# Optimization experiments

Measured on AMD Instinct MI355X. Metric: run time of the kernel, lower is better.

The kernel has to match this reference:

```python
import math
import jax, jax.numpy as jnp
import numpy as np

B, C_IN, S = 8, 1024, 2048
KEY_DIM, OUT_DIM = 512, 1024


def setup_inputs() -> dict:
    key = jax.random.key(0)
    ks = jax.random.split(key, 7)
    scale_in = 1.0 / math.sqrt(C_IN)
    return {
        "x": jax.random.normal(ks[0], (B, C_IN, S), dtype=jnp.float32),
        # Conv1d kernel_size=1 weights stored as (out_ch, in_ch)
        "wq": jax.random.uniform(ks[1], (KEY_DIM, C_IN), jnp.float32, -scale_in, scale_in),
        "bq": jax.random.uniform(ks[2], (KEY_DIM,), jnp.float32, -scale_in, scale_in),
        "wk": jax.random.uniform(ks[3], (KEY_DIM, C_IN), jnp.float32, -scale_in, scale_in),
        "bk": jax.random.uniform(ks[4], (KEY_DIM,), jnp.float32, -scale_in, scale_in),
        "wv": jax.random.uniform(ks[5], (OUT_DIM, C_IN), jnp.float32, -scale_in, scale_in),
        "bv": jax.random.uniform(ks[6], (OUT_DIM,), jnp.float32, -scale_in, scale_in),
    }


def reference(x, wq, bq, wk, bk, wv, bv):
    # x: (B, C, S). 1x1 Conv1d == per-position linear over channels.
    q = jnp.einsum("bcs,kc->bsk", x, wq) + bq            # (B, S, K)
    k = jnp.einsum("bcs,kc->bks", x, wk) + bk[:, None]   # (B, K, S)
    v = jnp.einsum("bcs,oc->bso", x, wv) + bv            # (B, S, O)
    scores = jnp.einsum("bsk,bkt->bst", q, k) / math.sqrt(KEY_DIM)  # (B, S, S)
    attention = jax.nn.softmax(scores, axis=-1)
    # out = (attn @ v) then transpose(1,2) -> (B, O, S)
    out = jnp.einsum("bst,bto->bos", attention, v)
    return out
```

## Files before the change

### kernel.cpp

```cpp
#include <hip/hip_runtime.h>
#include <hip/hip_bf16.h>
#include <math.h>

#define SEQ 2048
#define CIN 1024
#define KD  512
#define OD  1024
#define NB  8

typedef __attribute__((ext_vector_type(8))) short bf16x8;
typedef __attribute__((ext_vector_type(4))) float f32x4;

__device__ __forceinline__ short f2bs(float f) {
  unsigned u = __float_as_uint(f);
  unsigned r = (u + 0x7FFFu + ((u >> 16) & 1u)) >> 16;
  return (short)(r & 0xFFFFu);
}

__device__ __forceinline__ float bs2f(short s) {
  return __uint_as_float(((unsigned)(unsigned short)s) << 16);
}

__device__ __forceinline__ f32x4 mfma16(bf16x8 a, bf16x8 b, f32x4 c) {
  return __builtin_amdgcn_mfma_f32_16x16x32_bf16(a, b, c, 0, 0, 0);
}

__device__ __forceinline__ void gload16(const short* g, short* l) {
  __builtin_amdgcn_global_load_lds(
      (const __attribute__((address_space(1))) int*)g,
      (__attribute__((address_space(3))) int*)l, 16, 0, 0);
}

__global__ __launch_bounds__(256)
void cvt_ws(const float* __restrict__ in, short* __restrict__ out, int n) {
  int i = blockIdx.x * 256 + threadIdx.x;
  if (i < n) out[i] = f2bs(in[i]);
}

__global__ __launch_bounds__(256)
void transpose_cvt(const float* __restrict__ x, short* __restrict__ xt) {
  __shared__ float t[32][33];
  const int b = blockIdx.z;
  const int s0 = blockIdx.x * 32;
  const int c0 = blockIdx.y * 32;
  const int tx = threadIdx.x & 31;
  const int ty = threadIdx.x >> 5;
  const float* xb = x + (long)b * CIN * SEQ;
  #pragma unroll
  for (int i = 0; i < 32; i += 8)
    t[ty + i][tx] = xb[(long)(c0 + ty + i) * SEQ + s0 + tx];
  __syncthreads();
  short* xtb = xt + (long)b * SEQ * CIN;
  #pragma unroll
  for (int i = 0; i < 32; i += 8)
    xtb[(long)(s0 + ty + i) * CIN + c0 + tx] = f2bs(t[tx][ty + i]);
}

template<int BIAS_MODE, int OUT_BF16, int COLSCALE>
__global__ __launch_bounds__(256, 2)
void gemm_nt(const short* __restrict__ A, const short* __restrict__ Bm,
             const float* __restrict__ bias, const float* __restrict__ cs,
             void* __restrict__ C, int M, int N, int K,
             long sAb, long sBb, long sCb, float alpha) {
  __shared__ short lA[128 * 32];
  __shared__ short lB[128 * 32];
  const int bz = blockIdx.z;
  const long m0 = (long)blockIdx.y * 128;
  const long n0 = (long)blockIdx.x * 128;
  const short* Ab = A + (long)bz * sAb;
  const short* Bb = Bm + (long)bz * sBb;
  const int tid = threadIdx.x;
  const int lid = tid & 63;
  const int w = tid >> 6;
  const int wr = w >> 1, wc = w & 1;
  const int lr = lid & 15, kg = lid >> 4;
  const int srow = tid >> 2;
  const int scol = (tid & 3) * 8;

  f32x4 acc[4][4];
  #pragma unroll
  for (int i = 0; i < 4; i++)
    #pragma unroll
    for (int j = 0; j < 4; j++)
      acc[i][j] = f32x4{0.f, 0.f, 0.f, 0.f};

  for (int k0 = 0; k0 < K; k0 += 32) {
    __syncthreads();
    gload16(&Ab[(m0 + srow) * K + k0 + scol],      &lA[tid * 8]);
    gload16(&Ab[(m0 + 64 + srow) * K + k0 + scol], &lA[2048 + tid * 8]);
    gload16(&Bb[(n0 + srow) * K + k0 + scol],      &lB[tid * 8]);
    gload16(&Bb[(n0 + 64 + srow) * K + k0 + scol], &lB[2048 + tid * 8]);
    __syncthreads();
    bf16x8 af[4], bfr[4];
    #pragma unroll
    for (int mi = 0; mi < 4; mi++)
      af[mi] = *(const bf16x8*)&lA[(wr * 64 + mi * 16 + lr) * 32 + kg * 8];
    #pragma unroll
    for (int ni = 0; ni < 4; ni++)
      bfr[ni] = *(const bf16x8*)&lB[(wc * 64 + ni * 16 + lr) * 32 + kg * 8];
    #pragma unroll
    for (int mi = 0; mi < 4; mi++)
      #pragma unroll
      for (int ni = 0; ni < 4; ni++)
        acc[mi][ni] = mfma16(af[mi], bfr[ni], acc[mi][ni]);
  }

  #pragma unroll
  for (int mi = 0; mi < 4; mi++) {
    const long rowb = m0 + wr * 64 + mi * 16 + kg * 4;
    #pragma unroll
    for (int ni = 0; ni < 4; ni++) {
      const long col = n0 + wc * 64 + ni * 16 + lr;
      const float bc = (BIAS_MODE == 1) ? bias[col] : 0.f;
      const float sc = COLSCALE ? cs[(long)bz * SEQ + col] : 1.0f;
      #pragma unroll
      for (int r = 0; r < 4; r++) {
        float v = acc[mi][ni][r] * alpha + bc;
        if (BIAS_MODE == 2) v += bias[rowb + r];
        if (COLSCALE) v *= sc;
        const long idx = (long)bz * sCb + (rowb + r) * N + col;
        if (OUT_BF16) ((short*)C)[idx] = f2bs(v);
        else          ((float*)C)[idx] = v;
      }
    }
  }
}

__global__ __launch_bounds__(256, 2)
void attn_exp(const short* __restrict__ Q, const short* __restrict__ Km,
              short* __restrict__ E) {
  const float SCALE = 0.044194173824159216f;
  __shared__ short lA[128 * 32];
  __shared__ short lB[128 * 32];
  const int bz = blockIdx.z;
  const long q0 = (long)blockIdx.y * 128;
  const long t0 = (long)blockIdx.x * 128;
  const short* Qb = Q + (long)bz * SEQ * KD;
  const short* Kb = Km + (long)bz * SEQ * KD;
  const int tid = threadIdx.x;
  const int lid = tid & 63;
  const int w = tid >> 6;
  const int wr = w >> 1, wc = w & 1;
  const int lr = lid & 15, kg = lid >> 4;
  const int srow = tid >> 2;
  const int scol = (tid & 3) * 8;

  f32x4 acc[4][4];
  #pragma unroll
  for (int i = 0; i < 4; i++)
    #pragma unroll
    for (int j = 0; j < 4; j++)
      acc[i][j] = f32x4{0.f, 0.f, 0.f, 0.f};

  for (int k0 = 0; k0 < KD; k0 += 32) {
    __syncthreads();
    gload16(&Qb[(q0 + srow) * KD + k0 + scol],      &lA[tid * 8]);
    gload16(&Qb[(q0 + 64 + srow) * KD + k0 + scol], &lA[2048 + tid * 8]);
    gload16(&Kb[(t0 + srow) * KD + k0 + scol],      &lB[tid * 8]);
    gload16(&Kb[(t0 + 64 + srow) * KD + k0 + scol], &lB[2048 + tid * 8]);
    __syncthreads();
    bf16x8 af[4], bfr[4];
    #pragma unroll
    for (int mi = 0; mi < 4; mi++)
      af[mi] = *(const bf16x8*)&lA[(wr * 64 + mi * 16 + lr) * 32 + kg * 8];
    #pragma unroll
    for (int ni = 0; ni < 4; ni++)
      bfr[ni] = *(const bf16x8*)&lB[(wc * 64 + ni * 16 + lr) * 32 + kg * 8];
    #pragma unroll
    for (int mi = 0; mi < 4; mi++)
      #pragma unroll
      for (int ni = 0; ni < 4; ni++)
        acc[mi][ni] = mfma16(af[mi], bfr[ni], acc[mi][ni]);
  }

  short* Eb = E + (long)bz * SEQ * SEQ;
  #pragma unroll
  for (int mi = 0; mi < 4; mi++) {
    #pragma unroll
    for (int r = 0; r < 4; r++) {
      const long row = q0 + wr * 64 + mi * 16 + kg * 4 + r;
      #pragma unroll
      for (int ni = 0; ni < 4; ni++) {
        const long col = t0 + wc * 64 + ni * 16 + lr;
        Eb[row * SEQ + col] = f2bs(__expf(acc[mi][ni][r] * SCALE));
      }
    }
  }
}

__global__ __launch_bounds__(256)
void rowsum_recip(const short* __restrict__ E, float* __restrict__ linv) {
  const long row = (long)blockIdx.x * 4 + (threadIdx.x >> 6);
  const int lane = threadIdx.x & 63;
  const short* er = E + row * SEQ;
  float s = 0.f;
  #pragma unroll
  for (int i = 0; i < 4; i++) {
    bf16x8 v = *(const bf16x8*)&er[i * 512 + lane * 8];
    #pragma unroll
    for (int j = 0; j < 8; j++) s += bs2f(v[j]);
  }
  #pragma unroll
  for (int st = 1; st < 64; st <<= 1) s += __shfl_xor(s, st);
  if (lane == 0) linv[row] = 1.0f / s;
}

extern "C" void kernel_launch(void* const* d_in, const int* in_sizes, int n_in,
                              void* d_out, int out_size, void* d_ws, size_t ws_size,
                              hipStream_t stream) {
  (void)in_sizes; (void)n_in; (void)out_size; (void)ws_size;
  const float* x  = (const float*)d_in[0];
  const float* wq = (const float*)d_in[1];
  const float* bq = (const float*)d_in[2];
  const float* wk = (const float*)d_in[3];
  const float* bk = (const float*)d_in[4];
  const float* wv = (const float*)d_in[5];
  const float* bv = (const float*)d_in[6];

  char* ws = (char*)d_ws;
  short* XT = (short*)ws;
  short* E4 = (short*)ws;
  size_t off = (size_t)NB * SEQ * CIN * 2;
  short* Qb   = (short*)(ws + off); off += (size_t)NB * SEQ * KD * 2;
  short* Kb   = (short*)(ws + off); off += (size_t)NB * SEQ * KD * 2;
  short* Vb   = (short*)(ws + off); off += (size_t)NB * OD * SEQ * 2;
  float* linv = (float*)(ws + off); off += (size_t)4 * SEQ * 4;
  short* wqb  = (short*)(ws + off); off += (size_t)KD * CIN * 2;
  short* wkb  = (short*)(ws + off); off += (size_t)KD * CIN * 2;
  short* wvb  = (short*)(ws + off); off += (size_t)OD * CIN * 2;

  cvt_ws<<<dim3((KD * CIN + 255) / 256), 256, 0, stream>>>(wq, wqb, KD * CIN);
  cvt_ws<<<dim3((KD * CIN + 255) / 256), 256, 0, stream>>>(wk, wkb, KD * CIN);
  cvt_ws<<<dim3((OD * CIN + 255) / 256), 256, 0, stream>>>(wv, wvb, OD * CIN);

  transpose_cvt<<<dim3(SEQ / 32, CIN / 32, NB), 256, 0, stream>>>(x, XT);

  gemm_nt<1, 1, 0><<<dim3(KD / 128, SEQ / 128, NB), 256, 0, stream>>>(
      XT, wqb, bq, nullptr, Qb, SEQ, KD, CIN, (long)SEQ * CIN, 0, (long)SEQ * KD, 1.0f);
  gemm_nt<1, 1, 0><<<dim3(KD / 128, SEQ / 128, NB), 256, 0, stream>>>(
      XT, wkb, bk, nullptr, Kb, SEQ, KD, CIN, (long)SEQ * CIN, 0, (long)SEQ * KD, 1.0f);
  gemm_nt<2, 1, 0><<<dim3(SEQ / 128, OD / 128, NB), 256, 0, stream>>>(
      wvb, XT, bv, nullptr, Vb, OD, SEQ, CIN, 0, (long)SEQ * CIN, (long)OD * SEQ, 1.0f);

  for (int cb = 0; cb < NB; cb += 4) {
    attn_exp<<<dim3(SEQ / 128, SEQ / 128, 4), 256, 0, stream>>>(
        Qb + (long)cb * SEQ * KD, Kb + (long)cb * SEQ * KD, E4);
    rowsum_recip<<<dim3(4 * SEQ / 4), 256, 0, stream>>>(E4, linv);
    gemm_nt<0, 0, 1><<<dim3(SEQ / 128, OD / 128, 4), 256, 0, stream>>>(
        Vb + (long)cb * OD * SEQ, E4, nullptr, linv,
        (float*)d_out + (long)cb * OD * SEQ, OD, SEQ, SEQ,
        (long)OD * SEQ, (long)SEQ * SEQ, (long)OD * SEQ, 1.0f);
  }
}
```

Measured before the change: 399.9 us.

## Fuse Q/K projections, deepen K-tile to 64, batch all attention chunks

Doubles the LDS K-tile from 32 to 64 in both the GEMM and the attention-score kernels, halving the number of barrier pairs per K loop. Concatenates the wq and wk weights and biases so a single GEMM produces an interleaved QK buffer with row stride 1024, which attn_exp reads directly. When the workspace is large enough, all 8 batches go through the attention stage in one launch each instead of two chunks of 4. The cost is more LDS per block, which may lower occupancy, and a larger workspace requirement, with a fallback to the chunked path when the workspace is too small.

```diff
diff --git a/kernel.cpp b/kernel.cpp
--- a/kernel.cpp
+++ b/kernel.cpp
@@ -62,8 +62,8 @@
              const float* __restrict__ bias, const float* __restrict__ cs,
              void* __restrict__ C, int M, int N, int K,
              long sAb, long sBb, long sCb, float alpha) {
-  __shared__ short lA[128 * 32];
-  __shared__ short lB[128 * 32];
+  __shared__ short lA[128 * 64];
+  __shared__ short lB[128 * 64];
   const int bz = blockIdx.z;
   const long m0 = (long)blockIdx.y * 128;
   const long n0 = (long)blockIdx.x * 128;
@@ -74,8 +74,8 @@
   const int w = tid >> 6;
   const int wr = w >> 1, wc = w & 1;
   const int lr = lid & 15, kg = lid >> 4;
-  const int srow = tid >> 2;
-  const int scol = (tid & 3) * 8;
+  const int srow = tid >> 3;
+  const int scol = (tid & 7) * 8;
 
   f32x4 acc[4][4];
   #pragma unroll
@@ -84,25 +84,29 @@
     for (int j = 0; j < 4; j++)
       acc[i][j] = f32x4{0.f, 0.f, 0.f, 0.f};
 
-  for (int k0 = 0; k0 < K; k0 += 32) {
-    __syncthreads();
-    gload16(&Ab[(m0 + srow) * K + k0 + scol],      &lA[tid * 8]);
-    gload16(&Ab[(m0 + 64 + srow) * K + k0 + scol], &lA[2048 + tid * 8]);
-    gload16(&Bb[(n0 + srow) * K + k0 + scol],      &lB[tid * 8]);
-    gload16(&Bb[(n0 + 64 + srow) * K + k0 + scol], &lB[2048 + tid * 8]);
-    __syncthreads();
-    bf16x8 af[4], bfr[4];
-    #pragma unroll
-    for (int mi = 0; mi < 4; mi++)
-      af[mi] = *(const bf16x8*)&lA[(wr * 64 + mi * 16 + lr) * 32 + kg * 8];
-    #pragma unroll
-    for (int ni = 0; ni < 4; ni++)
-      bfr[ni] = *(const bf16x8*)&lB[(wc * 64 + ni * 16 + lr) * 32 + kg * 8];
-    #pragma unroll
-    for (int mi = 0; mi < 4; mi++)
+  for (int k0 = 0; k0 < K; k0 += 64) {
+    __syncthreads();
+    #pragma unroll
+    for (int i = 0; i < 4; i++) {
+      gload16(&Ab[(m0 + i * 32 + srow) * K + k0 + scol], &lA[i * 2048 + tid * 8]);
+      gload16(&Bb[(n0 + i * 32 + srow) * K + k0 + scol], &lB[i * 2048 + tid * 8]);
+    }
+    __syncthreads();
+    #pragma unroll
+    for (int kk = 0; kk < 2; kk++) {
+      bf16x8 af[4], bfr[4];
+      #pragma unroll
+      for (int mi = 0; mi < 4; mi++)
+        af[mi] = *(const bf16x8*)&lA[(wr * 64 + mi * 16 + lr) * 64 + kk * 32 + kg * 8];
       #pragma unroll
       for (int ni = 0; ni < 4; ni++)
-        acc[mi][ni] = mfma16(af[mi], bfr[ni], acc[mi][ni]);
+        bfr[ni] = *(const bf16x8*)&lB[(wc * 64 + ni * 16 + lr) * 64 + kk * 32 + kg * 8];
+      #pragma unroll
+      for (int mi = 0; mi < 4; mi++)
+        #pragma unroll
+        for (int ni = 0; ni < 4; ni++)
+          acc[mi][ni] = mfma16(af[mi], bfr[ni], acc[mi][ni]);
+    }
   }
 
   #pragma unroll
@@ -126,24 +130,25 @@
   }
 }
 
+#define LDQK 1024
 __global__ __launch_bounds__(256, 2)
 void attn_exp(const short* __restrict__ Q, const short* __restrict__ Km,
               short* __restrict__ E) {
   const float SCALE = 0.044194173824159216f;
-  __shared__ short lA[128 * 32];
-  __shared__ short lB[128 * 32];
+  __shared__ short lA[128 * 64];
+  __shared__ short lB[128 * 64];
   const int bz = blockIdx.z;
   const long q0 = (long)blockIdx.y * 128;
   const long t0 = (long)blockIdx.x * 128;
-  const short* Qb = Q + (long)bz * SEQ * KD;
-  const short* Kb = Km + (long)bz * SEQ * KD;
+  const short* Qb = Q + (long)bz * SEQ * LDQK;
+  const short* Kb = Km + (long)bz * SEQ * LDQK;
   const int tid = threadIdx.x;
   const int lid = tid & 63;
   const int w = tid >> 6;
   const int wr = w >> 1, wc = w & 1;
   const int lr = lid & 15, kg = lid >> 4;
-  const int srow = tid >> 2;
-  const int scol = (tid & 3) * 8;
+  const int srow = tid >> 3;
+  const int scol = (tid & 7) * 8;
 
   f32x4 acc[4][4];
   #pragma unroll
@@ -152,25 +157,29 @@
     for (int j = 0; j < 4; j++)
       acc[i][j] = f32x4{0.f, 0.f, 0.f, 0.f};
 
-  for (int k0 = 0; k0 < KD; k0 += 32) {
-    __syncthreads();
-    gload16(&Qb[(q0 + srow) * KD + k0 + scol],      &lA[tid * 8]);
-    gload16(&Qb[(q0 + 64 + srow) * KD + k0 + scol], &lA[2048 + tid * 8]);
-    gload16(&Kb[(t0 + srow) * KD + k0 + scol],      &lB[tid * 8]);
-    gload16(&Kb[(t0 + 64 + srow) * KD + k0 + scol], &lB[2048 + tid * 8]);
-    __syncthreads();
-    bf16x8 af[4], bfr[4];
-    #pragma unroll
-    for (int mi = 0; mi < 4; mi++)
-      af[mi] = *(const bf16x8*)&lA[(wr * 64 + mi * 16 + lr) * 32 + kg * 8];
-    #pragma unroll
-    for (int ni = 0; ni < 4; ni++)
-      bfr[ni] = *(const bf16x8*)&lB[(wc * 64 + ni * 16 + lr) * 32 + kg * 8];
-    #pragma unroll
-    for (int mi = 0; mi < 4; mi++)
+  for (int k0 = 0; k0 < KD; k0 += 64) {
+    __syncthreads();
+    #pragma unroll
+    for (int i = 0; i < 4; i++) {
+      gload16(&Qb[(q0 + i * 32 + srow) * LDQK + k0 + scol], &lA[i * 2048 + tid * 8]);
+      gload16(&Kb[(t0 + i * 32 + srow) * LDQK + k0 + scol], &lB[i * 2048 + tid * 8]);
+    }
+    __syncthreads();
+    #pragma unroll
+    for (int kk = 0; kk < 2; kk++) {
+      bf16x8 af[4], bfr[4];
+      #pragma unroll
+      for (int mi = 0; mi < 4; mi++)
+        af[mi] = *(const bf16x8*)&lA[(wr * 64 + mi * 16 + lr) * 64 + kk * 32 + kg * 8];
       #pragma unroll
       for (int ni = 0; ni < 4; ni++)
-        acc[mi][ni] = mfma16(af[mi], bfr[ni], acc[mi][ni]);
+        bfr[ni] = *(const bf16x8*)&lB[(wc * 64 + ni * 16 + lr) * 64 + kk * 32 + kg * 8];
+      #pragma unroll
+      for (int mi = 0; mi < 4; mi++)
+        #pragma unroll
+        for (int ni = 0; ni < 4; ni++)
+          acc[mi][ni] = mfma16(af[mi], bfr[ni], acc[mi][ni]);
+    }
   }
 
   short* Eb = E + (long)bz * SEQ * SEQ;
@@ -208,7 +217,7 @@
 extern "C" void kernel_launch(void* const* d_in, const int* in_sizes, int n_in,
                               void* d_out, int out_size, void* d_ws, size_t ws_size,
                               hipStream_t stream) {
-  (void)in_sizes; (void)n_in; (void)out_size; (void)ws_size;
+  (void)in_sizes; (void)n_in; (void)out_size;
   const float* x  = (const float*)d_in[0];
   const float* wq = (const float*)d_in[1];
   const float* bq = (const float*)d_in[2];
@@ -217,37 +226,45 @@
   const float* wv = (const float*)d_in[5];
   const float* bv = (const float*)d_in[6];
 
+  const size_t SZ_XT  = (size_t)NB * SEQ * CIN * 2;
+  const size_t SZ_E8  = (size_t)NB * SEQ * SEQ * 2;
+  const size_t SZ_QK  = (size_t)NB * SEQ * 1024 * 2;
+  const size_t SZ_V   = (size_t)NB * OD * SEQ * 2;
+  const size_t SZ_TAIL = (size_t)NB * SEQ * 4 + 4096 + 2 * (size_t)1024 * 1024 * 2 + 4096;
+  const bool full = ws_size >= (SZ_E8 + SZ_QK + SZ_V + SZ_TAIL);
+  const size_t region0 = full ? SZ_E8 : SZ_XT;
+
   char* ws = (char*)d_ws;
-  short* XT = (short*)ws;
-  short* E4 = (short*)ws;
-  size_t off = (size_t)NB * SEQ * CIN * 2;
-  short* Qb   = (short*)(ws + off); off += (size_t)NB * SEQ * KD * 2;
-  short* Kb   = (short*)(ws + off); off += (size_t)NB * SEQ * KD * 2;
-  short* Vb   = (short*)(ws + off); off += (size_t)NB * OD * SEQ * 2;
-  float* linv = (float*)(ws + off); off += (size_t)4 * SEQ * 4;
-  short* wqb  = (short*)(ws + off); off += (size_t)KD * CIN * 2;
-  short* wkb  = (short*)(ws + off); off += (size_t)KD * CIN * 2;
+  short* XT  = (short*)ws;
+  short* Ebf = (short*)ws;
+  size_t off = region0;
+  short* QKb  = (short*)(ws + off); off += SZ_QK;
+  short* Vb   = (short*)(ws + off); off += SZ_V;
+  float* linv = (float*)(ws + off); off += (size_t)NB * SEQ * 4;
+  float* bqk  = (float*)(ws + off); off += 4096;
+  short* wqkb = (short*)(ws + off); off += (size_t)1024 * CIN * 2;
   short* wvb  = (short*)(ws + off); off += (size_t)OD * CIN * 2;
 
-  cvt_ws<<<dim3((KD * CIN + 255) / 256), 256, 0, stream>>>(wq, wqb, KD * CIN);
-  cvt_ws<<<dim3((KD * CIN + 255) / 256), 256, 0, stream>>>(wk, wkb, KD * CIN);
+  cvt_ws<<<dim3((KD * CIN + 255) / 256), 256, 0, stream>>>(wq, wqkb, KD * CIN);
+  cvt_ws<<<dim3((KD * CIN + 255) / 256), 256, 0, stream>>>(wk, wqkb + (size_t)KD * CIN, KD * CIN);
   cvt_ws<<<dim3((OD * CIN + 255) / 256), 256, 0, stream>>>(wv, wvb, OD * CIN);
+  hipMemcpyAsync(bqk, bq, KD * 4, hipMemcpyDeviceToDevice, stream);
+  hipMemcpyAsync(bqk + KD, bk, KD * 4, hipMemcpyDeviceToDevice, stream);
 
   transpose_cvt<<<dim3(SEQ / 32, CIN / 32, NB), 256, 0, stream>>>(x, XT);
 
-  gemm_nt<1, 1, 0><<<dim3(KD / 128, SEQ / 128, NB), 256, 0, stream>>>(
-      XT, wqb, bq, nullptr, Qb, SEQ, KD, CIN, (long)SEQ * CIN, 0, (long)SEQ * KD, 1.0f);
-  gemm_nt<1, 1, 0><<<dim3(KD / 128, SEQ / 128, NB), 256, 0, stream>>>(
-      XT, wkb, bk, nullptr, Kb, SEQ, KD, CIN, (long)SEQ * CIN, 0, (long)SEQ * KD, 1.0f);
+  gemm_nt<1, 1, 0><<<dim3(1024 / 128, SEQ / 128, NB), 256, 0, stream>>>(
+      XT, wqkb, bqk, nullptr, QKb, SEQ, 1024, CIN, (long)SEQ * CIN, 0, (long)SEQ * 1024, 1.0f);
   gemm_nt<2, 1, 0><<<dim3(SEQ / 128, OD / 128, NB), 256, 0, stream>>>(
       wvb, XT, bv, nullptr, Vb, OD, SEQ, CIN, 0, (long)SEQ * CIN, (long)OD * SEQ, 1.0f);
 
-  for (int cb = 0; cb < NB; cb += 4) {
-    attn_exp<<<dim3(SEQ / 128, SEQ / 128, 4), 256, 0, stream>>>(
-        Qb + (long)cb * SEQ * KD, Kb + (long)cb * SEQ * KD, E4);
-    rowsum_recip<<<dim3(4 * SEQ / 4), 256, 0, stream>>>(E4, linv);
-    gemm_nt<0, 0, 1><<<dim3(SEQ / 128, OD / 128, 4), 256, 0, stream>>>(
-        Vb + (long)cb * OD * SEQ, E4, nullptr, linv,
+  const int CB = full ? NB : 4;
+  for (int cb = 0; cb < NB; cb += CB) {
+    attn_exp<<<dim3(SEQ / 128, SEQ / 128, CB), 256, 0, stream>>>(
+        QKb + (long)cb * SEQ * 1024, QKb + (long)cb * SEQ * 1024 + KD, Ebf);
+    rowsum_recip<<<dim3(CB * SEQ / 4), 256, 0, stream>>>(Ebf, linv);
+    gemm_nt<0, 0, 1><<<dim3(SEQ / 128, OD / 128, CB), 256, 0, stream>>>(
+        Vb + (long)cb * OD * SEQ, Ebf, nullptr, linv,
         (float*)d_out + (long)cb * OD * SEQ, OD, SEQ, SEQ,
         (long)OD * SEQ, (long)SEQ * SEQ, (long)OD * SEQ, 1.0f);
   }
```

New measurement: 402.3 us. About the same (+0.6%).
